# Kernel tuning notes

Measured on AMD Instinct MI355X. Metric: run time of the kernel, lower is better.

Reference implementation:

```python
import jax, jax.numpy as jnp
import numpy as np

B, C, H, W, D = 4, 256, 16, 16, 16
N = H * W * D          # 4096 tokens == input_size
HEADS, P = 8, 64       # num_heads, proj_size
EPS_LN, EPS_BN, NEG_SLOPE = 1e-5, 1e-5, 0.01


def setup_inputs() -> dict:
    key = jax.random.key(0)
    ks = jax.random.split(key, 10)
    s = 0.02
    rn = lambda k, shp: (s * jax.random.normal(k, shp)).astype(jnp.float32)
    return {
        "x": jax.random.normal(ks[0], (B, C, H, W, D), jnp.float32),
        "gamma": 1e-6 * jnp.ones((C,), jnp.float32),
        "ln_w": jnp.ones((C,), jnp.float32),
        "ln_b": jnp.zeros((C,), jnp.float32),
        "qkvv_w": rn(ks[1], (4 * C, C)),          # Linear(C, 4C), bias=False
        "ef_w": rn(ks[2], (P, N)),                 # shared E == F projection
        "ef_b": jnp.zeros((P,), jnp.float32),
        "temp": jnp.ones((HEADS, 1, 1), jnp.float32),
        "temp2": jnp.ones((HEADS, 1, 1), jnp.float32),
        "op1_w": rn(ks[3], (C // 2, C)),
        "op1_b": jnp.zeros((C // 2,), jnp.float32),
        "op2_w": rn(ks[4], (C // 2, C)),
        "op2_b": jnp.zeros((C // 2,), jnp.float32),
        "conv1_w": rn(ks[5], (C, C, 3, 3, 3)),     # UnetResBlock convs, bias=False
        "bn1_w": jnp.ones((C,), jnp.float32),
        "bn1_b": jnp.zeros((C,), jnp.float32),
        "conv2_w": rn(ks[6], (C, C, 3, 3, 3)),
        "bn2_w": jnp.ones((C,), jnp.float32),
        "bn2_b": jnp.zeros((C,), jnp.float32),
        "conv8_w": rn(ks[7], (C, C, 1, 1, 1)),     # nn.Conv3d 1x1x1, bias=True
        "conv8_b": jnp.zeros((C,), jnp.float32),
    }


def _l2norm(t):  # torch F.normalize(dim=-1)
    n = jnp.sqrt(jnp.sum(t * t, axis=-1, keepdims=True))
    return t / jnp.maximum(n, 1e-12)


def _conv3d(x, w, pad):
    return jax.lax.conv_general_dilated(
        x, w, window_strides=(1, 1, 1), padding=[(pad, pad)] * 3,
        dimension_numbers=("NCDHW", "OIDHW", "NCDHW"))


def _bn(x, w, b):  # BatchNorm3d, training-mode batch stats, biased var
    mu = jnp.mean(x, axis=(0, 2, 3, 4), keepdims=True)
    var = jnp.mean((x - mu) ** 2, axis=(0, 2, 3, 4), keepdims=True)
    xh = (x - mu) / jnp.sqrt(var + EPS_BN)
    return xh * w[None, :, None, None, None] + b[None, :, None, None, None]


def _lrelu(x):
    return jnp.where(x >= 0, x, NEG_SLOPE * x)


def _epa(xs, qkvv_w, ef_w, ef_b, temp, temp2, op1_w, op1_b, op2_w, op2_b):
    Bq, Nq, Cq = xs.shape
    d = Cq // HEADS
    qkvv = (xs @ qkvv_w.T).reshape(Bq, Nq, 4, HEADS, d)
    qkvv = jnp.transpose(qkvv, (2, 0, 3, 1, 4))         # (4,B,h,N,d)
    q, k, v_ca, v_sa = qkvv[0], qkvv[1], qkvv[2], qkvv[3]
    q = jnp.swapaxes(q, -2, -1)                          # (B,h,d,N)
    k = jnp.swapaxes(k, -2, -1)
    v_ca = jnp.swapaxes(v_ca, -2, -1)
    v_sa = jnp.swapaxes(v_sa, -2, -1)
    k_proj = k @ ef_w.T + ef_b                           # (B,h,d,P)
    v_sa_proj = v_sa @ ef_w.T + ef_b                     # (B,h,d,P)
    qn = _l2norm(q)
    kn = _l2norm(k)
    # channel attention: (B,h,d,d)
    attn_ca = jax.nn.softmax(jnp.einsum("bhdn,bhen->bhde", qn, kn) * temp, axis=-1)
    x_ca = jnp.einsum("bhde,bhen->bhdn", attn_ca, v_ca)  # (B,h,d,N)
    x_ca = jnp.transpose(x_ca, (0, 3, 1, 2)).reshape(Bq, Nq, Cq)
    # spatial attention with projected K/V: (B,h,N,P)
    attn_sa = jax.nn.softmax(jnp.einsum("bhdn,bhdp->bhnp", qn, k_proj) * temp2, axis=-1)
    x_sa = jnp.einsum("bhnp,bhdp->bhnd", attn_sa, v_sa_proj)   # (B,h,N,d)
    # faithful to source: permute(0,3,1,2) then reshape(B,N,C)
    x_sa = jnp.transpose(x_sa, (0, 3, 1, 2)).reshape(Bq, Nq, Cq)
    x_sa = x_sa @ op1_w.T + op1_b
    x_ca = x_ca @ op2_w.T + op2_b
    return jnp.concatenate((x_sa, x_ca), axis=-1)


def reference(x, gamma, ln_w, ln_b, qkvv_w, ef_w, ef_b, temp, temp2,
              op1_w, op1_b, op2_w, op2_b, conv1_w, bn1_w, bn1_b,
              conv2_w, bn2_w, bn2_b, conv8_w, conv8_b):
    Bq, Cq, Hq, Wq, Dq = x.shape
    Nq = Hq * Wq * Dq
    xs = jnp.transpose(x.reshape(Bq, Cq, Nq), (0, 2, 1))       # (B,N,C)
    mu = jnp.mean(xs, axis=-1, keepdims=True)
    var = jnp.mean((xs - mu) ** 2, axis=-1, keepdims=True)
    xn = (xs - mu) / jnp.sqrt(var + EPS_LN) * ln_w + ln_b
    attn = xs + gamma * _epa(xn, qkvv_w, ef_w, ef_b, temp, temp2,
                             op1_w, op1_b, op2_w, op2_b)
    attn_skip = jnp.transpose(attn.reshape(Bq, Hq, Wq, Dq, Cq), (0, 4, 1, 2, 3))
    # UnetResBlock (identity shortcut: same channels, stride 1)
    h1 = _lrelu(_bn(_conv3d(attn_skip, conv1_w, 1), bn1_w, bn1_b))
    h2 = _bn(_conv3d(h1, conv2_w, 1), bn2_w, bn2_b)
    conv_out = _lrelu(h2 + attn_skip)
    # conv8: Dropout3d (identity in eval) + 1x1x1 conv with bias
    c8 = _conv3d(conv_out, conv8_w, 0) + conv8_b[None, :, None, None, None]
    return attn_skip + c8
```

## Files before the change

kernel.cpp:

```cpp
#include <hip/hip_runtime.h>

#define B_ 4
#define C_ 256
#define N_ 4096

typedef unsigned short u16;
typedef __attribute__((ext_vector_type(8))) short short8_t;
typedef __attribute__((ext_vector_type(4))) float f32x4;

__device__ __forceinline__ u16 bf16r(float f) {
  unsigned u = __float_as_uint(f);
  return (u16)((u + 0x7FFFu + ((u >> 16) & 1u)) >> 16);
}
__device__ __forceinline__ float bf2f(u16 u) {
  return __uint_as_float(((unsigned)u) << 16);
}

__device__ __forceinline__ void g2l16(const u16* g, u16* l) {
  __builtin_amdgcn_global_load_lds((const __attribute__((address_space(1))) void*)g,
                                   (__attribute__((address_space(3))) void*)l, 16, 0, 0);
}

__device__ __forceinline__ int f4(int x) { return (x ^ (x >> 2)) & 3; }

__global__ __launch_bounds__(256) void k_ln(const float* __restrict__ x,
                                            const float* __restrict__ ln_w,
                                            const float* __restrict__ ln_b,
                                            u16* __restrict__ xnb) {
  __shared__ float tile[32][260];
  __shared__ float s_mu[32], s_rs[32];
  int b = blockIdx.y, n0 = blockIdx.x * 32, tid = threadIdx.x;
  for (int idx = tid; idx < 32 * 256; idx += 256) {
    int nl = idx & 31, c = idx >> 5;
    tile[nl][c] = x[((size_t)(b * C_ + c)) * N_ + n0 + nl];
  }
  __syncthreads();
  int token = tid >> 3, sub = tid & 7;
  float s = 0.f, sq = 0.f;
  for (int j = 0; j < 32; ++j) {
    float v = tile[token][sub + j * 8];
    s += v; sq += v * v;
  }
  for (int o = 1; o < 8; o <<= 1) { s += __shfl_xor(s, o); sq += __shfl_xor(sq, o); }
  if (sub == 0) {
    float mu = s * (1.f / 256.f);
    float var = sq * (1.f / 256.f) - mu * mu;
    s_mu[token] = mu;
    s_rs[token] = rsqrtf(var + 1e-5f);
  }
  __syncthreads();
  int c = tid;
  float lw = ln_w[c], lb = ln_b[c];
  for (int k = 0; k < 32; ++k) {
    float v = (tile[k][c] - s_mu[k]) * s_rs[k] * lw + lb;
    xnb[((size_t)(b * N_ + n0 + k)) * 256 + c] = bf16r(v);
  }
}

__global__ __launch_bounds__(256) void k_pack(const float* __restrict__ w,
                                              u16* __restrict__ dst,
                                              int ntap, int K) {
  int tid = threadIdx.x;
  int tile = blockIdx.x;
  int tap = tile % ntap; int tmp = tile / ntap; int Kt = K >> 5;
  int k0 = tmp % Kt; int ot = tmp / Kt;
  u16* td = dst + (size_t)tile * 4096;
  int m = tid >> 1;
  int kb = (tid & 1) * 16;
  int fm = f4(m);
  #pragma unroll
  for (int j = 0; j < 16; ++j) {
    int k = kb + j;
    float v = w[((size_t)(ot * 128 + m) * K + k0 * 32 + k) * ntap + tap];
    td[m * 32 + (((k >> 3) ^ fm) << 3) + (k & 7)] = bf16r(v);
  }
}

__global__ __launch_bounds__(256) void k_packA(const float* __restrict__ w,
                                               u16* __restrict__ dst) {
  int tid = threadIdx.x;
  int tile = blockIdx.x;
  int tap = tile % 27; int tmp = tile / 27;
  int k0 = tmp & 7; int ot = tmp >> 3;
  u16* td = dst + (size_t)tile * 4096;
  int m = tid >> 1;
  int kb = (tid & 1) * 16;
  #pragma unroll
  for (int j = 0; j < 16; ++j) {
    int k = kb + j;
    float v = w[((size_t)(ot * 128 + m) * 256 + k0 * 32 + k) * 27 + tap];
    td[m * 32 + k] = bf16r(v);
  }
}

__global__ __launch_bounds__(64) void k_packef(const float* __restrict__ ef,
                                               u16* __restrict__ dst) {
  int k0 = blockIdx.x, m = threadIdx.x, fm = f4(m);
  u16* td = dst + (size_t)k0 * 2048;
  #pragma unroll
  for (int k = 0; k < 32; ++k)
    td[m * 32 + (((k >> 3) ^ fm) << 3) + (k & 7)] = bf16r(ef[(size_t)m * 4096 + k0 * 32 + k]);
}

__global__ __launch_bounds__(256) void k_gemm(const u16* __restrict__ xnb,
                                              const u16* __restrict__ qpack,
                                              u16* __restrict__ qct,
                                              float* __restrict__ sbuf) {
  __shared__ alignas(16) u16 At[4096];
  __shared__ alignas(16) u16 Bt[4096];
  __shared__ alignas(16) u16 Tt[128 * 136];
  int tid = threadIdx.x, l = tid & 63, w = tid >> 6;
  int wm = w >> 1, wn = w & 1;
  int kg = l >> 4;
  int tok0 = blockIdx.x * 128, oct = blockIdx.y;
  int b = tok0 >> 12;
  int aoff[4], boff[4];
  #pragma unroll
  for (int r = 0; r < 4; ++r) {
    int m = wm * 64 + r * 16 + (l & 15);
    aoff[r] = m * 32 + ((kg ^ f4(m)) << 3);
    int o = wn * 64 + r * 16 + (l & 15);
    boff[r] = o * 32 + ((kg ^ f4(o)) << 3);
  }
  f32x4 acc[4][4];
  #pragma unroll
  for (int r = 0; r < 4; ++r)
    #pragma unroll
    for (int jt = 0; jt < 4; ++jt)
      acc[r][jt] = (f32x4){0.f, 0.f, 0.f, 0.f};
  for (int k0 = 0; k0 < 8; ++k0) {
    __syncthreads();
    #pragma unroll
    for (int it = 0; it < 2; ++it) {
      int slot = it * 256 + tid;
      int row = slot >> 2, cp = slot & 3;
      int cig = cp ^ f4(row);
      g2l16(xnb + ((size_t)(tok0 + row) * 256 + k0 * 32 + cig * 8),
            &At[(it * 256 + (tid & 192)) * 8]);
    }
    const u16* qb = qpack + ((size_t)(oct * 8 + k0) << 12);
    #pragma unroll
    for (int it = 0; it < 2; ++it)
      g2l16(qb + (it * 256 + tid) * 8, &Bt[(it * 256 + (tid & 192)) * 8]);
    __syncthreads();
    short8_t av[4], bv[4];
    #pragma unroll
    for (int r = 0; r < 4; ++r) av[r] = *(const short8_t*)&At[aoff[r]];
    #pragma unroll
    for (int jt = 0; jt < 4; ++jt) bv[jt] = *(const short8_t*)&Bt[boff[jt]];
    #pragma unroll
    for (int r = 0; r < 4; ++r)
      #pragma unroll
      for (int jt = 0; jt < 4; ++jt)
        acc[r][jt] = __builtin_amdgcn_mfma_f32_16x16x32_bf16(av[r], bv[jt], acc[r][jt], 0, 0, 0);
  }
  if (oct < 4) {
    #pragma unroll
    for (int jt = 0; jt < 4; ++jt) {
      float ss = 0.f;
      #pragma unroll
      for (int r = 0; r < 4; ++r)
        #pragma unroll
        for (int reg = 0; reg < 4; ++reg)
          ss += acc[r][jt][reg] * acc[r][jt][reg];
      ss += __shfl_xor(ss, 16);
      ss += __shfl_xor(ss, 32);
      if ((l >> 4) == 0) {
        int oc = oct * 128 + wn * 64 + jt * 16 + (l & 15);
        atomicAdd(&sbuf[(oc >> 8) * 1024 + b * 256 + (oc & 255)], ss);
      }
    }
  }
  #pragma unroll
  for (int r = 0; r < 4; ++r) {
    int tokl = wm * 64 + r * 16 + ((l >> 4) << 2);
    #pragma unroll
    for (int jt = 0; jt < 4; ++jt) {
      int ocl = wn * 64 + jt * 16 + (l & 15);
      ushort4 h4;
      h4.x = bf16r(acc[r][jt][0]);
      h4.y = bf16r(acc[r][jt][1]);
      h4.z = bf16r(acc[r][jt][2]);
      h4.w = bf16r(acc[r][jt][3]);
      *(ushort4*)&Tt[ocl * 136 + tokl] = h4;
    }
  }
  __syncthreads();
  int n0 = tok0 & 4095;
  #pragma unroll
  for (int i = 0; i < 8; ++i) {
    int s = i * 256 + tid;
    int row = s >> 4;
    int col = (s & 15) * 8;
    *(int4*)&qct[((size_t)(b * 1024 + oct * 128 + row)) * 4096 + n0 + col] =
        *(const int4*)&Tt[row * 136 + col];
  }
}

__global__ __launch_bounds__(256) void k_rsq(const float* __restrict__ sbuf,
                                             float* __restrict__ inv) {
  int i = blockIdx.x * 256 + threadIdx.x;
  inv[i] = 1.f / fmaxf(sqrtf(sbuf[i]), 1e-12f);
}

__global__ __launch_bounds__(256) void k_kvproj_m(const u16* __restrict__ qct,
                                                  const u16* __restrict__ efp,
                                                  float* __restrict__ kvpart) {
  __shared__ alignas(16) u16 At[16384];
  __shared__ alignas(16) u16 Bt[8192];
  int tid = threadIdx.x, l = tid & 63, w = tid >> 6;
  int mt = blockIdx.x, b = blockIdx.y, kz = blockIdx.z;
  int ccb = (mt < 2) ? (256 + mt * 128) : (768 + (mt - 2) * 128);
  int kg = l >> 4;
  int aoff[2], boff[4];
  #pragma unroll
  for (int r = 0; r < 2; ++r) {
    int m = w * 32 + r * 16 + (l & 15);
    aoff[r] = m * 32 + ((kg ^ f4(m)) << 3);
  }
  #pragma unroll
  for (int jt = 0; jt < 4; ++jt) {
    int o = jt * 16 + (l & 15);
    boff[jt] = o * 32 + ((kg ^ f4(o)) << 3);
  }
  f32x4 acc[2][4];
  #pragma unroll
  for (int r = 0; r < 2; ++r)
    #pragma unroll
    for (int jt = 0; jt < 4; ++jt) acc[r][jt] = (f32x4){0.f, 0.f, 0.f, 0.f};
  for (int k0 = kz * 8; k0 < kz * 8 + 8; ++k0) {
    __syncthreads();
    #pragma unroll
    for (int it = 0; it < 8; ++it) {
      int slot = it * 256 + tid;
      int sub = slot >> 9, r = (slot >> 2) & 127, cp = slot & 3;
      g2l16(qct + ((size_t)(b * 1024 + ccb + r)) * 4096 + k0 * 128 + sub * 32 + ((cp ^ f4(r)) << 3),
            &At[(it * 256 + (tid & 192)) * 8]);
    }
    #pragma unroll
    for (int it = 0; it < 4; ++it) {
      int slot = it * 256 + tid;
      g2l16(efp + (size_t)k0 * 8192 + slot * 8, &Bt[(it * 256 + (tid & 192)) * 8]);
    }
    __syncthreads();
    #pragma unroll
    for (int sub = 0; sub < 4; ++sub) {
      short8_t av[2], bv[4];
      #pragma unroll
      for (int r = 0; r < 2; ++r) av[r] = *(const short8_t*)&At[sub * 4096 + aoff[r]];
      #pragma unroll
      for (int jt = 0; jt < 4; ++jt) bv[jt] = *(const short8_t*)&Bt[sub * 2048 + boff[jt]];
      #pragma unroll
      for (int r = 0; r < 2; ++r)
        #pragma unroll
        for (int jt = 0; jt < 4; ++jt)
          acc[r][jt] = __builtin_amdgcn_mfma_f32_16x16x32_bf16(av[r], bv[jt], acc[r][jt], 0, 0, 0);
    }
  }
  int kv = mt >> 1;
  float* outd = kvpart + (size_t)kv * 524288 + (size_t)kz * 131072;
  #pragma unroll
  for (int r = 0; r < 2; ++r) {
    int cbase = (mt & 1) * 128 + w * 32 + r * 16 + ((l >> 4) << 2);
    #pragma unroll
    for (int jt = 0; jt < 4; ++jt) {
      int p = jt * 16 + (l & 15);
      #pragma unroll
      for (int reg = 0; reg < 4; ++reg) {
        int cc = cbase + reg;
        outd[((size_t)(b * 8 + (cc >> 5))) * 2048 + (cc & 31) * 64 + p] = acc[r][jt][reg];
      }
    }
  }
}

__global__ __launch_bounds__(256) void k_kvred(const float* __restrict__ kvpart,
                                               const float* __restrict__ ef_b,
                                               float* __restrict__ kproj,
                                               float* __restrict__ vproj) {
  int kv = blockIdx.y;
  int i = (blockIdx.x * 256 + threadIdx.x) * 4;
  const float* p = kvpart + (size_t)kv * 524288 + i;
  float4 a0 = *(const float4*)&p[0];
  float4 a1 = *(const float4*)&p[131072];
  float4 a2 = *(const float4*)&p[262144];
  float4 a3 = *(const float4*)&p[393216];
  int pp = i & 63;
  float4 o;
  o.x = a0.x + a1.x + a2.x + a3.x + ef_b[pp];
  o.y = a0.y + a1.y + a2.y + a3.y + ef_b[pp + 1];
  o.z = a0.z + a1.z + a2.z + a3.z + ef_b[pp + 2];
  o.w = a0.w + a1.w + a2.w + a3.w + ef_b[pp + 3];
  float* outd = kv ? vproj : kproj;
  *(float4*)&outd[i] = o;
}

__global__ __launch_bounds__(256) void k_attnca_p(const u16* __restrict__ qct,
                                                  float* __restrict__ Spp) {
  __shared__ u16 Qs[32][520], Ks[32][520];
  int bh = blockIdx.x, ns = blockIdx.y;
  int b = bh >> 3, h = bh & 7;
  int tid = threadIdx.x;
  int n0 = ns * 512;
  for (int idx = tid; idx < 2048; idx += 256) {
    int r = idx >> 6, ch = (idx & 63) * 8;
    *(int4*)&Qs[r][ch] = *(const int4*)&qct[((size_t)(b * 1024 + h * 32 + r)) * 4096 + n0 + ch];
    *(int4*)&Ks[r][ch] = *(const int4*)&qct[((size_t)(b * 1024 + 256 + h * 32 + r)) * 4096 + n0 + ch];
  }
  __syncthreads();
  int r = tid >> 3, sub = tid & 7;
  float a0 = 0.f, a1 = 0.f, a2 = 0.f, a3 = 0.f;
  for (int nb = 0; nb < 512; nb += 8) {
    short8_t q8 = *(const short8_t*)&Qs[r][nb];
    short8_t k0 = *(const short8_t*)&Ks[sub][nb];
    short8_t k1 = *(const short8_t*)&Ks[sub + 8][nb];
    short8_t k2 = *(const short8_t*)&Ks[sub + 16][nb];
    short8_t k3 = *(const short8_t*)&Ks[sub + 24][nb];
    #pragma unroll
    for (int j = 0; j < 8; ++j) {
      float qv = bf2f((u16)q8[j]);
      a0 += qv * bf2f((u16)k0[j]);
      a1 += qv * bf2f((u16)k1[j]);
      a2 += qv * bf2f((u16)k2[j]);
      a3 += qv * bf2f((u16)k3[j]);
    }
  }
  float* sp = Spp + (size_t)ns * 32768 + (size_t)bh * 1024 + r * 32;
  sp[sub] = a0;
  sp[sub + 8] = a1;
  sp[sub + 16] = a2;
  sp[sub + 24] = a3;
}

__global__ __launch_bounds__(64) void k_casm(const float* __restrict__ Spp,
                                             const float* __restrict__ inv,
                                             const float* __restrict__ temp,
                                             float* __restrict__ Aca) {
  int bh = blockIdx.x, b = bh >> 3, h = bh & 7;
  int tid = threadIdx.x;
  if (tid < 32) {
    float qiv = inv[b * 256 + h * 32 + tid];
    float tmp = temp[h];
    float vals[32];
    #pragma unroll
    for (int e = 0; e < 32; ++e) vals[e] = 0.f;
    for (int ns = 0; ns < 8; ++ns) {
      const float* sp = Spp + (size_t)ns * 32768 + (size_t)bh * 1024 + tid * 32;
      #pragma unroll
      for (int e4 = 0; e4 < 32; e4 += 4) {
        float4 v4 = *(const float4*)&sp[e4];
        vals[e4] += v4.x; vals[e4 + 1] += v4.y;
        vals[e4 + 2] += v4.z; vals[e4 + 3] += v4.w;
      }
    }
    float m = -1e30f;
    #pragma unroll
    for (int e = 0; e < 32; ++e) {
      float s = vals[e] * qiv * inv[1024 + b * 256 + h * 32 + e] * tmp;
      vals[e] = s;
      m = fmaxf(m, s);
    }
    float ssum = 0.f;
    #pragma unroll
    for (int e = 0; e < 32; ++e) { vals[e] = __expf(vals[e] - m); ssum += vals[e]; }
    float is = 1.f / ssum;
    #pragma unroll
    for (int e = 0; e < 32; ++e) Aca[((size_t)bh * 32 + tid) * 32 + e] = vals[e] * is;
  }
}

__global__ __launch_bounds__(256) void k_xca(const u16* __restrict__ qct,
                                             const float* __restrict__ Aca,
                                             u16* __restrict__ xca_b) {
  __shared__ float A[32][33];
  __shared__ float vt[32][129];
  int n0 = blockIdx.x * 128;
  int h = blockIdx.y, b = blockIdx.z;
  int bh = b * 8 + h;
  int tid = threadIdx.x;
  for (int idx = tid; idx < 1024; idx += 256) A[idx >> 5][idx & 31] = Aca[(size_t)bh * 1024 + idx];
  int e = tid >> 3, ns = (tid & 7) * 16;
  const u16* src = qct + ((size_t)(b * 1024 + 512 + h * 32 + e)) * 4096 + n0 + ns;
  #pragma unroll
  for (int j4 = 0; j4 < 16; j4 += 4) {
    ushort4 u = *(const ushort4*)&src[j4];
    vt[e][ns + j4] = bf2f(u.x);
    vt[e][ns + j4 + 1] = bf2f(u.y);
    vt[e][ns + j4 + 2] = bf2f(u.z);
    vt[e][ns + j4 + 3] = bf2f(u.w);
  }
  __syncthreads();
  int nl = tid & 127, dg = (tid >> 7) * 16;
  float acc[16] = {};
  for (int ee = 0; ee < 32; ++ee) {
    float v = vt[ee][nl];
    #pragma unroll
    for (int j = 0; j < 16; ++j) acc[j] += A[dg + j][ee] * v;
  }
  u16* outp = xca_b + ((size_t)(b * N_ + n0 + nl)) * 256 + h * 32 + dg;
  #pragma unroll
  for (int j = 0; j < 16; ++j) outp[j] = bf16r(acc[j]);
}

__global__ __launch_bounds__(256) void k_attnsa(const u16* __restrict__ qct,
                                                const float* __restrict__ kproj,
                                                const float* __restrict__ vproj,
                                                const float* __restrict__ inv,
                                                const float* __restrict__ temp2,
                                                u16* __restrict__ xsa_b) {
  __shared__ float kp[32][64], vp[32][64], qi[32];
  __shared__ u16 qt[32][260];
  __shared__ float ot[32][257];
  int bx = blockIdx.x;
  int h = blockIdx.y, b = blockIdx.z;
  int bh = b * 8 + h;
  int tid = threadIdx.x;
  for (int idx = tid; idx < 2048; idx += 256) {
    kp[idx >> 6][idx & 63] = kproj[(size_t)bh * 2048 + idx];
    vp[idx >> 6][idx & 63] = vproj[(size_t)bh * 2048 + idx];
  }
  if (tid < 32) qi[tid] = inv[bh * 32 + tid];
  {
    int row = tid >> 3, ch = (tid & 7) * 32;
    const u16* src = qct + ((size_t)(b * 1024 + h * 32 + row)) * 4096 + bx * 256 + ch;
    *(int4*)&qt[row][ch] = *(const int4*)&src[0];
    *(int4*)&qt[row][ch + 8] = *(const int4*)&src[8];
    *(int4*)&qt[row][ch + 16] = *(const int4*)&src[16];
    *(int4*)&qt[row][ch + 24] = *(const int4*)&src[24];
  }
  __syncthreads();
  float q[32];
  #pragma unroll
  for (int d = 0; d < 32; ++d) q[d] = bf2f(qt[d][tid]) * qi[d];
  float t2 = temp2[h];
  float l[64];
  #pragma unroll
  for (int p = 0; p < 64; ++p) {
    float s = 0;
    #pragma unroll
    for (int d = 0; d < 32; ++d) s += q[d] * kp[d][p];
    l[p] = s * t2;
  }
  float m = -1e30f;
  #pragma unroll
  for (int p = 0; p < 64; ++p) m = fmaxf(m, l[p]);
  float ssum = 0;
  #pragma unroll
  for (int p = 0; p < 64; ++p) { l[p] = __expf(l[p] - m); ssum += l[p]; }
  float is = 1.f / ssum;
  float o[32] = {};
  #pragma unroll
  for (int p = 0; p < 64; ++p) {
    float wv = l[p] * is;
    #pragma unroll
    for (int d = 0; d < 32; ++d) o[d] += wv * vp[d][p];
  }
  #pragma unroll
  for (int d = 0; d < 32; ++d) ot[d][tid] = o[d];
  __syncthreads();
  #pragma unroll
  for (int i = 0; i < 4; ++i) {
    int s = i * 256 + tid;
    int d = s >> 5;
    int c0 = (s & 31) * 8;
    ushort4 u0, u1;
    u0.x = bf16r(ot[d][c0]);     u0.y = bf16r(ot[d][c0 + 1]);
    u0.z = bf16r(ot[d][c0 + 2]); u0.w = bf16r(ot[d][c0 + 3]);
    u1.x = bf16r(ot[d][c0 + 4]); u1.y = bf16r(ot[d][c0 + 5]);
    u1.z = bf16r(ot[d][c0 + 6]); u1.w = bf16r(ot[d][c0 + 7]);
    u16* dst = xsa_b + (size_t)b * N_ * 256 + (size_t)(d * 128 + h * 16 + bx) * 256 + c0;
    *(ushort4*)&dst[0] = u0;
    *(ushort4*)&dst[4] = u1;
  }
}

__global__ __launch_bounds__(256) void k_opcatm(const u16* __restrict__ xsa_b,
                                                const u16* __restrict__ xca_b,
                                                const float* __restrict__ x,
                                                const float* __restrict__ gamma,
                                                const u16* __restrict__ oppack,
                                                const float* __restrict__ op1_b,
                                                const float* __restrict__ op2_b,
                                                float* __restrict__ attn_skip,
                                                u16* __restrict__ xt1) {
  __shared__ alignas(16) u16 At[4096];
  __shared__ alignas(16) u16 Bt[4096];
  __shared__ alignas(16) float Ttf[128 * 133];
  __shared__ alignas(16) u16 rb[128 * 136];
  int tid = threadIdx.x, l = tid & 63, w = tid >> 6;
  int wm = w >> 1, wn = w & 1;
  int kg = l >> 4;
  int tok0 = blockIdx.x * 128, oct = blockIdx.y;
  int b = tok0 >> 12;
  const u16* src = oct ? xca_b : xsa_b;
  int aoff[4], boff[4];
  #pragma unroll
  for (int r = 0; r < 4; ++r) {
    int m = wm * 64 + r * 16 + (l & 15);
    aoff[r] = m * 32 + ((kg ^ f4(m)) << 3);
    int o = wn * 64 + r * 16 + (l & 15);
    boff[r] = o * 32 + ((kg ^ f4(o)) << 3);
  }
  f32x4 acc[4][4];
  #pragma unroll
// ... 168 lines not shown
    #pragma unroll
    for (int r = 0; r < 4; ++r) av[0][r] = *(const short8_t*)(at + r * 512);
    #pragma unroll
    for (int r = 0; r < 4; ++r) av[1][r] = *(const short8_t*)(at + 4096 + r * 512);
    #pragma unroll
    for (int r = 0; r < 4; ++r) av[2][r] = *(const short8_t*)(at + 8192 + r * 512);
    #pragma unroll
    for (int jt = 0; jt < 4; ++jt) {
      bv[0][jt] = *(const short8_t*)&Xb[(cellc[jt] - 197) * 8];
      bv[1][jt] = *(const short8_t*)&Xb[(cellc[jt] - 196) * 8];
    }
    #pragma unroll
    for (int t = 0; t < 4; ++t) CONV_TAP(t);
    if (step < 3) {
      const int nd = (step + 1) & 1;
      #pragma unroll
      for (int bk = 0; bk < 2; ++bk)
        #pragma unroll
        for (int i = 0; i < 4; ++i) {
          const u16* p = ((okm >> i) & 1) ? (xp[i] + ((bk * 4 + step + 1) << 5)) : zg;
          g2l16(p, &Xs[bk][nd][(i * 256 + (tid & 192)) * 8]);
        }
    }
    #pragma unroll
    for (int t = 4; t < 27; ++t) CONV_TAP(t);
    __syncthreads();
  }
#undef CONV_TAP

  f32x4* red = (f32x4*)&Xs[0][0][0];
  if (ks == 1) {
    #pragma unroll
    for (int r = 0; r < 4; ++r)
      #pragma unroll
      for (int jt = 0; jt < 4; ++jt)
        red[(r * 4 + jt) * 128 + wm * 64 + l] = acc[r][jt];
  }
  __syncthreads();
  if (ks == 0) {
    #pragma unroll
    for (int r = 0; r < 4; ++r)
      #pragma unroll
      for (int jt = 0; jt < 4; ++jt) {
        f32x4 o = red[(r * 4 + jt) * 128 + wm * 64 + l];
        acc[r][jt][0] += o[0]; acc[r][jt][1] += o[1];
        acc[r][jt][2] += o[2]; acc[r][jt][3] += o[3];
      }
    #pragma unroll
    for (int r = 0; r < 4; ++r) {
      int co = cot * 128 + wm * 64 + r * 16 + ((l >> 4) << 2);
      #pragma unroll
      for (int reg = 0; reg < 4; ++reg) {
        float sv = 0.f, qv = 0.f;
        #pragma unroll
        for (int jt = 0; jt < 4; ++jt) {
          float v = acc[r][jt][reg];
          sv += v; qv += v * v;
        }
        #pragma unroll
        for (int o = 1; o < 16; o <<= 1) {
          sv += __shfl_xor(sv, o);
          qv += __shfl_xor(qv, o);
        }
        if ((l & 15) == 0) {
          atomicAdd(&bnsum[co + reg], sv);
          atomicAdd(&bnsq[co + reg], qv);
        }
      }
      #pragma unroll
      for (int jt = 0; jt < 4; ++jt) {
        int c = jt * 16 + (l & 15);
        int n = (h0 + (c >> 4)) * 256 + (w0 + ((c >> 2) & 3)) * 16 + (d0 + (c & 3));
        ushort4 h4;
        h4.x = bf16r(acc[r][jt][0]);
        h4.y = bf16r(acc[r][jt][1]);
        h4.z = bf16r(acc[r][jt][2]);
        h4.w = bf16r(acc[r][jt][3]);
        *(ushort4*)&out[((size_t)(b * N_ + n)) * 256 + co] = h4;
      }
    }
  }
}

__global__ __launch_bounds__(256) void k_bnfin(const float* __restrict__ bnsum,
                                               const float* __restrict__ bnsq,
                                               float* __restrict__ mu,
                                               float* __restrict__ rstd) {
  int c = threadIdx.x;
  float m = bnsum[c] * (1.f / 16384.f);
  float var = bnsq[c] * (1.f / 16384.f) - m * m;
  mu[c] = m;
  rstd[c] = rsqrtf(var + 1e-5f);
}

__global__ __launch_bounds__(256) void k_bnelt(const u16* __restrict__ src,
                                               const float* __restrict__ mu,
                                               const float* __restrict__ rstd,
                                               const float* __restrict__ w,
                                               const float* __restrict__ bb,
                                               u16* __restrict__ dst) {
  __shared__ float sc[256], sh[256];
  int tid = threadIdx.x;
  float scv = rstd[tid] * w[tid];
  sc[tid] = scv;
  sh[tid] = bb[tid] - mu[tid] * scv;
  __syncthreads();
  size_t base = (size_t)blockIdx.x * 64 * 256;
  #pragma unroll
  for (int i = 0; i < 8; ++i) {
    int s = i * 256 + tid;
    int c0 = (s & 31) * 8;
    size_t off = base + (size_t)(s >> 5) * 256 + c0;
    int4 v4 = *(const int4*)&src[off];
    u16* pu = (u16*)&v4;
    #pragma unroll
    for (int j = 0; j < 8; ++j) {
      float v = bf2f(pu[j]) * sc[c0 + j] + sh[c0 + j];
      pu[j] = bf16r(v >= 0.f ? v : 0.01f * v);
    }
    *(int4*)&dst[off] = v4;
  }
}

__global__ __launch_bounds__(256) void k_bn2fuse(const u16* __restrict__ c2o,
                                                 const float* __restrict__ askip,
                                                 const float* __restrict__ mu2,
                                                 const float* __restrict__ rs2,
                                                 const float* __restrict__ bnw,
                                                 const float* __restrict__ bnb,
                                                 u16* __restrict__ cvo) {
  __shared__ float sc[256], sh[256];
  __shared__ float at_[32][260];
  int n0 = blockIdx.x * 32, b = blockIdx.y, tid = threadIdx.x;
  float scv = rs2[tid] * bnw[tid];
  sc[tid] = scv;
  sh[tid] = bnb[tid] - mu2[tid] * scv;
  {
    int c = tid;
    const float* ar = askip + ((size_t)(b * 256 + c)) * 4096 + n0;
    #pragma unroll
    for (int nl = 0; nl < 32; ++nl) at_[nl][c] = ar[nl];
  }
  __syncthreads();
  #pragma unroll
  for (int i = 0; i < 4; ++i) {
    int s = i * 256 + tid;
    int row = s >> 5, c0 = (s & 31) * 8;
    size_t off = ((size_t)(b * N_ + n0 + row)) * 256 + c0;
    int4 v4 = *(const int4*)&c2o[off];
    u16* pu = (u16*)&v4;
    #pragma unroll
    for (int j = 0; j < 8; ++j) {
      int c = c0 + j;
      float v = bf2f(pu[j]) * sc[c] + sh[c] + at_[row][c];
      pu[j] = bf16r(v >= 0.f ? v : 0.01f * v);
    }
    *(int4*)&cvo[off] = v4;
  }
}

__global__ __launch_bounds__(256) void k_conv8m(const u16* __restrict__ cvo,
                                                const u16* __restrict__ w8p,
                                                const float* __restrict__ b8,
                                                const float* __restrict__ skip,
                                                float* __restrict__ out) {
  __shared__ alignas(16) u16 At[4096];
  __shared__ alignas(16) u16 Bt[4096];
  __shared__ alignas(16) float Ts[128 * 132];
  int tid = threadIdx.x, l = tid & 63, w = tid >> 6;
  int wm = w >> 1, wn = w & 1;
  int kg = l >> 4;
  int tok0 = blockIdx.x * 128, oct = blockIdx.y;
  int b = tok0 >> 12;
  int aoff[4], boff[4];
  #pragma unroll
  for (int r = 0; r < 4; ++r) {
    int m = wm * 64 + r * 16 + (l & 15);
    aoff[r] = m * 32 + ((kg ^ f4(m)) << 3);
    int o = wn * 64 + r * 16 + (l & 15);
    boff[r] = o * 32 + ((kg ^ f4(o)) << 3);
  }
  f32x4 acc[4][4];
  #pragma unroll
  for (int r = 0; r < 4; ++r)
    #pragma unroll
    for (int jt = 0; jt < 4; ++jt)
      acc[r][jt] = (f32x4){0.f, 0.f, 0.f, 0.f};
  for (int k0 = 0; k0 < 8; ++k0) {
    __syncthreads();
    #pragma unroll
    for (int it = 0; it < 2; ++it) {
      int slot = it * 256 + tid;
      int row = slot >> 2, cp = slot & 3;
      int cig = cp ^ f4(row);
      g2l16(cvo + ((size_t)(tok0 + row) * 256 + k0 * 32 + cig * 8),
            &At[(it * 256 + (tid & 192)) * 8]);
    }
    const u16* qb = w8p + ((size_t)(oct * 8 + k0) << 12);
    #pragma unroll
    for (int it = 0; it < 2; ++it)
      g2l16(qb + (it * 256 + tid) * 8, &Bt[(it * 256 + (tid & 192)) * 8]);
    __syncthreads();
    short8_t av[4], bv[4];
    #pragma unroll
    for (int r = 0; r < 4; ++r) av[r] = *(const short8_t*)&At[aoff[r]];
    #pragma unroll
    for (int jt = 0; jt < 4; ++jt) bv[jt] = *(const short8_t*)&Bt[boff[jt]];
    #pragma unroll
    for (int r = 0; r < 4; ++r)
      #pragma unroll
      for (int jt = 0; jt < 4; ++jt)
        acc[r][jt] = __builtin_amdgcn_mfma_f32_16x16x32_bf16(av[r], bv[jt], acc[r][jt], 0, 0, 0);
  }
  #pragma unroll
  for (int r = 0; r < 4; ++r) {
    int tokl = wm * 64 + r * 16 + ((l >> 4) << 2);
    #pragma unroll
    for (int jt = 0; jt < 4; ++jt) {
      int ocl = wn * 64 + jt * 16 + (l & 15);
      *(float4*)&Ts[ocl * 132 + tokl] =
          (float4){acc[r][jt][0], acc[r][jt][1], acc[r][jt][2], acc[r][jt][3]};
    }
  }
  __syncthreads();
  int n0l = tok0 & 4095;
  #pragma unroll
  for (int i = 0; i < 16; ++i) {
    int s = i * 256 + tid;
    int row = s >> 5;
    int c4 = (s & 31) * 4;
    int oc = oct * 128 + row;
    size_t base = ((size_t)(b * 256 + oc)) * 4096 + n0l + c4;
    float4 s4 = *(const float4*)&skip[base];
    float bias = b8[oc];
    const float* tp = &Ts[row * 132 + c4];
    float4 o4;
    o4.x = s4.x + bias + tp[0];
    o4.y = s4.y + bias + tp[1];
    o4.z = s4.z + bias + tp[2];
    o4.w = s4.w + bias + tp[3];
    *(float4*)&out[base] = o4;
  }
}

extern "C" void kernel_launch(void* const* d_in, const int* in_sizes, int n_in,
                              void* d_out, int out_size, void* d_ws, size_t ws_size,
                              hipStream_t stream) {
  const float* x       = (const float*)d_in[0];
  const float* gamma   = (const float*)d_in[1];
  const float* ln_w    = (const float*)d_in[2];
  const float* ln_b    = (const float*)d_in[3];
  const float* qkvv_w  = (const float*)d_in[4];
  const float* ef_w    = (const float*)d_in[5];
  const float* ef_b    = (const float*)d_in[6];
  const float* temp    = (const float*)d_in[7];
  const float* temp2   = (const float*)d_in[8];
  const float* op1_w   = (const float*)d_in[9];
  const float* op1_b   = (const float*)d_in[10];
  const float* op2_w   = (const float*)d_in[11];
  const float* op2_b   = (const float*)d_in[12];
  const float* conv1_w = (const float*)d_in[13];
  const float* bn1_w   = (const float*)d_in[14];
  const float* bn1_b   = (const float*)d_in[15];
  const float* conv2_w = (const float*)d_in[16];
  const float* bn2_w   = (const float*)d_in[17];
  const float* bn2_b   = (const float*)d_in[18];
  const float* conv8_w = (const float*)d_in[19];
  const float* conv8_b = (const float*)d_in[20];

  float* ws = (float*)d_ws;
  const size_t M1 = 1u << 20;
  float* askip  = ws;
  u16*   xt1    = (u16*)(ws + 16 * M1);
  u16*   xnb    = (u16*)(ws + 18 * M1);
  float* kvpart = ws + 18 * M1;
  float* Spp    = ws + 19 * M1;
  u16*   xsa_b  = (u16*)(ws + 18 * M1);
  u16*   xca_b  = (u16*)(ws + 22 * M1);
  u16*   cvo    = (u16*)(ws + 22 * M1);
  u16*   qct    = (u16*)(ws + 24 * M1);
  u16*   apack1 = (u16*)(ws + 24 * M1);
  u16*   apack2 = (u16*)(ws + 25 * M1);
  u16*   c1o    = (u16*)(ws + 26 * M1);
  u16*   ht     = (u16*)(ws + 28 * M1);
  u16*   c2o    = (u16*)(ws + 30 * M1);
  float* sm     = ws + 32 * M1;
  float* sbuf   = sm;
  float* qkinv  = sbuf + 2048;
  float* kproj  = qkinv + 2048;
  float* vproj  = kproj + 65536;
  float* Sp     = vproj + 65536;
  float* bnacc  = Sp + 32768;
  float* zgu_f  = bnacc + 1024;
  u16*   zgu    = (u16*)zgu_f;
  float* Aca    = zgu_f + 128;
  float* mu1    = Aca + 32768;
  float* rs1    = mu1 + 256;
  float* mu2    = rs1 + 256;
  float* rs2    = mu2 + 256;
  u16*   qpack  = (u16*)(rs2 + 256);
  u16*   efpack = (u16*)(rs2 + 256 + 131072);
  u16*   w8pack = (u16*)(rs2 + 256 + 262144);
  u16*   oppack = (u16*)(rs2 + 256 + 262144 + 32768);

  hipMemsetAsync(sbuf, 0, 2048 * 4, stream);
  hipMemsetAsync(bnacc, 0, (1024 + 128) * 4, stream);
  k_pack<<<dim3(64), 256, 0, stream>>>(qkvv_w, qpack, 1, 256);
  k_pack<<<dim3(16), 256, 0, stream>>>(conv8_w, w8pack, 1, 256);
  k_pack<<<dim3(8), 256, 0, stream>>>(op1_w, oppack, 1, 256);
  k_pack<<<dim3(8), 256, 0, stream>>>(op2_w, oppack + 32768, 1, 256);
  k_packef<<<dim3(128), 64, 0, stream>>>(ef_w, efpack);
  k_ln<<<dim3(128, 4), 256, 0, stream>>>(x, ln_w, ln_b, xnb);
  k_gemm<<<dim3(128, 8), 256, 0, stream>>>(xnb, qpack, qct, sbuf);
  k_rsq<<<dim3(8), 256, 0, stream>>>(sbuf, qkinv);
  k_kvproj_m<<<dim3(4, 4, 4), 256, 0, stream>>>(qct, efpack, kvpart);
  k_kvred<<<dim3(64, 2), 256, 0, stream>>>(kvpart, ef_b, kproj, vproj);
  k_attnca_p<<<dim3(32, 8), 256, 0, stream>>>(qct, Spp);
  k_casm<<<dim3(32), 64, 0, stream>>>(Spp, qkinv, temp, Aca);
  k_xca<<<dim3(32, 8, 4), 256, 0, stream>>>(qct, Aca, xca_b);
  k_attnsa<<<dim3(16, 8, 4), 256, 0, stream>>>(qct, kproj, vproj, qkinv, temp2, xsa_b);
  k_opcatm<<<dim3(128, 2), 256, 0, stream>>>(xsa_b, xca_b, x, gamma, oppack, op1_b, op2_b, askip, xt1);
  k_packA<<<dim3(432), 256, 0, stream>>>(conv1_w, apack1);
  k_packA<<<dim3(432), 256, 0, stream>>>(conv2_w, apack2);
  k_conv3m<<<dim3(512), 256, 0, stream>>>(xt1, apack1, zgu, c1o, bnacc, bnacc + 256);
  k_bnfin<<<1, 256, 0, stream>>>(bnacc, bnacc + 256, mu1, rs1);
  k_bnelt<<<dim3(256), 256, 0, stream>>>(c1o, mu1, rs1, bn1_w, bn1_b, ht);
  k_conv3m<<<dim3(512), 256, 0, stream>>>(ht, apack2, zgu, c2o, bnacc + 512, bnacc + 768);
  k_bnfin<<<1, 256, 0, stream>>>(bnacc + 512, bnacc + 768, mu2, rs2);
  k_bn2fuse<<<dim3(128, 4), 256, 0, stream>>>(c2o, askip, mu2, rs2, bn2_w, bn2_b, cvo);
  k_conv8m<<<dim3(128, 2), 256, 0, stream>>>(cvo, w8pack, conv8_b, askip, (float*)d_out);
}
```

Baseline: 353.5 us.

## Merge weight-pack kernels and fold small reduction kernels into consumers

Combines all weight packing into one k_prepack launch and merges the two memsets into one. Removes the small kernels k_rsq, k_kvred, k_casm and k_bnfin by recomputing their results inside the consuming kernels (k_xca, k_attnsa, k_bnelt, k_bn2fuse). The workspace layout is rearranged so apack1/apack2 do not alias qct and can be packed up front. The intent is to cut launch count and serialization gaps, at the cost of redundant per-block recomputation such as the softmax and kv reduction in every k_xca block.

```diff
diff --git a/kernel.cpp b/kernel.cpp
--- a/kernel.cpp
+++ b/kernel.cpp
@@ -57,49 +57,60 @@
   }
 }
 
-__global__ __launch_bounds__(256) void k_pack(const float* __restrict__ w,
-                                              u16* __restrict__ dst,
-                                              int ntap, int K) {
-  int tid = threadIdx.x;
-  int tile = blockIdx.x;
-  int tap = tile % ntap; int tmp = tile / ntap; int Kt = K >> 5;
-  int k0 = tmp % Kt; int ot = tmp / Kt;
-  u16* td = dst + (size_t)tile * 4096;
-  int m = tid >> 1;
-  int kb = (tid & 1) * 16;
-  int fm = f4(m);
-  #pragma unroll
-  for (int j = 0; j < 16; ++j) {
-    int k = kb + j;
-    float v = w[((size_t)(ot * 128 + m) * K + k0 * 32 + k) * ntap + tap];
-    td[m * 32 + (((k >> 3) ^ fm) << 3) + (k & 7)] = bf16r(v);
-  }
-}
-
-__global__ __launch_bounds__(256) void k_packA(const float* __restrict__ w,
-                                               u16* __restrict__ dst) {
-  int tid = threadIdx.x;
-  int tile = blockIdx.x;
-  int tap = tile % 27; int tmp = tile / 27;
-  int k0 = tmp & 7; int ot = tmp >> 3;
-  u16* td = dst + (size_t)tile * 4096;
-  int m = tid >> 1;
-  int kb = (tid & 1) * 16;
-  #pragma unroll
-  for (int j = 0; j < 16; ++j) {
-    int k = kb + j;
-    float v = w[((size_t)(ot * 128 + m) * 256 + k0 * 32 + k) * 27 + tap];
-    td[m * 32 + k] = bf16r(v);
-  }
-}
-
-__global__ __launch_bounds__(64) void k_packef(const float* __restrict__ ef,
-                                               u16* __restrict__ dst) {
-  int k0 = blockIdx.x, m = threadIdx.x, fm = f4(m);
-  u16* td = dst + (size_t)k0 * 2048;
-  #pragma unroll
-  for (int k = 0; k < 32; ++k)
-    td[m * 32 + (((k >> 3) ^ fm) << 3) + (k & 7)] = bf16r(ef[(size_t)m * 4096 + k0 * 32 + k]);
+__global__ __launch_bounds__(256) void k_prepack(const float* __restrict__ qkvv_w,
+                                                 const float* __restrict__ conv8_w,
+                                                 const float* __restrict__ op1_w,
+                                                 const float* __restrict__ op2_w,
+                                                 const float* __restrict__ ef_w,
+                                                 const float* __restrict__ conv1_w,
+                                                 const float* __restrict__ conv2_w,
+                                                 u16* __restrict__ qpack,
+                                                 u16* __restrict__ w8pack,
+                                                 u16* __restrict__ oppack,
+                                                 u16* __restrict__ efpack,
+                                                 u16* __restrict__ apack1,
+                                                 u16* __restrict__ apack2) {
+  int bid = blockIdx.x, tid = threadIdx.x;
+  if (bid < 96) {
+    const float* w; u16* dst; int tile;
+    if (bid < 64)      { w = qkvv_w;  dst = qpack;          tile = bid; }
+    else if (bid < 80) { w = conv8_w; dst = w8pack;         tile = bid - 64; }
+    else if (bid < 88) { w = op1_w;   dst = oppack;         tile = bid - 80; }
+    else               { w = op2_w;   dst = oppack + 32768; tile = bid - 88; }
+    int k0 = tile & 7, ot = tile >> 3;
+    u16* td = dst + (size_t)tile * 4096;
+    int m = tid >> 1, kb = (tid & 1) * 16, fm = f4(m);
+    #pragma unroll
+    for (int j = 0; j < 16; ++j) {
+      int k = kb + j;
+      float v = w[(size_t)(ot * 128 + m) * 256 + k0 * 32 + k];
+      td[m * 32 + (((k >> 3) ^ fm) << 3) + (k & 7)] = bf16r(v);
+    }
+  } else if (bid < 224) {
+    int k0 = bid - 96;
+    int m = tid & 63, kq = tid >> 6, fm = f4(m);
+    u16* td = efpack + (size_t)k0 * 2048;
+    #pragma unroll
+    for (int kk = 0; kk < 8; ++kk) {
+      int k = kq * 8 + kk;
+      td[m * 32 + (((k >> 3) ^ fm) << 3) + (k & 7)] = bf16r(ef_w[(size_t)m * 4096 + k0 * 32 + k]);
+    }
+  } else {
+    int t = bid - 224;
+    const float* w = (t < 432) ? conv1_w : conv2_w;
+    u16* dst = (t < 432) ? apack1 : apack2;
+    int tile = (t < 432) ? t : t - 432;
+    int tap = tile % 27; int tmp = tile / 27;
+    int k0 = tmp & 7; int ot = tmp >> 3;
+    u16* td = dst + (size_t)tile * 4096;
+    int m = tid >> 1, kb = (tid & 1) * 16;
+    #pragma unroll
+    for (int j = 0; j < 16; ++j) {
+      int k = kb + j;
+      float v = w[((size_t)(ot * 128 + m) * 256 + k0 * 32 + k) * 27 + tap];
+      td[m * 32 + k] = bf16r(v);
+    }
+  }
 }
 
 __global__ __launch_bounds__(256) void k_gemm(const u16* __restrict__ xnb,
@@ -197,12 +208,6 @@
   }
 }
 
-__global__ __launch_bounds__(256) void k_rsq(const float* __restrict__ sbuf,
-                                             float* __restrict__ inv) {
-  int i = blockIdx.x * 256 + threadIdx.x;
-  inv[i] = 1.f / fmaxf(sqrtf(sbuf[i]), 1e-12f);
-}
-
 __global__ __launch_bounds__(256) void k_kvproj_m(const u16* __restrict__ qct,
                                                   const u16* __restrict__ efp,
                                                   float* __restrict__ kvpart) {
@@ -272,27 +277,6 @@
       }
     }
   }
-}
-
-__global__ __launch_bounds__(256) void k_kvred(const float* __restrict__ kvpart,
-                                               const float* __restrict__ ef_b,
-                                               float* __restrict__ kproj,
-                                               float* __restrict__ vproj) {
-  int kv = blockIdx.y;
-  int i = (blockIdx.x * 256 + threadIdx.x) * 4;
-  const float* p = kvpart + (size_t)kv * 524288 + i;
-  float4 a0 = *(const float4*)&p[0];
-  float4 a1 = *(const float4*)&p[131072];
-  float4 a2 = *(const float4*)&p[262144];
-  float4 a3 = *(const float4*)&p[393216];
-  int pp = i & 63;
-  float4 o;
-  o.x = a0.x + a1.x + a2.x + a3.x + ef_b[pp];
-  o.y = a0.y + a1.y + a2.y + a3.y + ef_b[pp + 1];
-  o.z = a0.z + a1.z + a2.z + a3.z + ef_b[pp + 2];
-  o.w = a0.w + a1.w + a2.w + a3.w + ef_b[pp + 3];
-  float* outd = kv ? vproj : kproj;
-  *(float4*)&outd[i] = o;
 }
 
 __global__ __launch_bounds__(256) void k_attnca_p(const u16* __restrict__ qct,
@@ -332,45 +316,10 @@
   sp[sub + 24] = a3;
 }
 
-__global__ __launch_bounds__(64) void k_casm(const float* __restrict__ Spp,
-                                             const float* __restrict__ inv,
+__global__ __launch_bounds__(256) void k_xca(const u16* __restrict__ qct,
+                                             const float* __restrict__ Spp,
+                                             const float* __restrict__ sbuf,
                                              const float* __restrict__ temp,
-                                             float* __restrict__ Aca) {
-  int bh = blockIdx.x, b = bh >> 3, h = bh & 7;
-  int tid = threadIdx.x;
-  if (tid < 32) {
-    float qiv = inv[b * 256 + h * 32 + tid];
-    float tmp = temp[h];
-    float vals[32];
-    #pragma unroll
-    for (int e = 0; e < 32; ++e) vals[e] = 0.f;
-    for (int ns = 0; ns < 8; ++ns) {
-      const float* sp = Spp + (size_t)ns * 32768 + (size_t)bh * 1024 + tid * 32;
-      #pragma unroll
-      for (int e4 = 0; e4 < 32; e4 += 4) {
-        float4 v4 = *(const float4*)&sp[e4];
-        vals[e4] += v4.x; vals[e4 + 1] += v4.y;
-        vals[e4 + 2] += v4.z; vals[e4 + 3] += v4.w;
-      }
-    }
-    float m = -1e30f;
-    #pragma unroll
-    for (int e = 0; e < 32; ++e) {
-      float s = vals[e] * qiv * inv[1024 + b * 256 + h * 32 + e] * tmp;
-      vals[e] = s;
-      m = fmaxf(m, s);
-    }
-    float ssum = 0.f;
-    #pragma unroll
-    for (int e = 0; e < 32; ++e) { vals[e] = __expf(vals[e] - m); ssum += vals[e]; }
-    float is = 1.f / ssum;
-    #pragma unroll
-    for (int e = 0; e < 32; ++e) Aca[((size_t)bh * 32 + tid) * 32 + e] = vals[e] * is;
-  }
-}
-
-__global__ __launch_bounds__(256) void k_xca(const u16* __restrict__ qct,
-                                             const float* __restrict__ Aca,
                                              u16* __restrict__ xca_b) {
   __shared__ float A[32][33];
   __shared__ float vt[32][129];
@@ -378,7 +327,36 @@
   int h = blockIdx.y, b = blockIdx.z;
   int bh = b * 8 + h;
   int tid = threadIdx.x;
-  for (int idx = tid; idx < 1024; idx += 256) A[idx >> 5][idx & 31] = Aca[(size_t)bh * 1024 + idx];
+  if (tid < 32) {
+    float qiv = 1.f / fmaxf(sqrtf(sbuf[b * 256 + h * 32 + tid]), 1e-12f);
+    float tmp = temp[h];
+    float vals[32];
+    #pragma unroll
+    for (int e = 0; e < 32; ++e) vals[e] = 0.f;
+    for (int ns = 0; ns < 8; ++ns) {
+      const float* sp = Spp + (size_t)ns * 32768 + (size_t)bh * 1024 + tid * 32;
+      #pragma unroll
+      for (int e4 = 0; e4 < 32; e4 += 4) {
+        float4 v4 = *(const float4*)&sp[e4];
+        vals[e4] += v4.x; vals[e4 + 1] += v4.y;
+        vals[e4 + 2] += v4.z; vals[e4 + 3] += v4.w;
+      }
+    }
+    float mx = -1e30f;
+    #pragma unroll
+    for (int e = 0; e < 32; ++e) {
+      float kiv = 1.f / fmaxf(sqrtf(sbuf[1024 + b * 256 + h * 32 + e]), 1e-12f);
+      float s = vals[e] * qiv * kiv * tmp;
+      vals[e] = s;
+      mx = fmaxf(mx, s);
+    }
+    float ssum = 0.f;
+    #pragma unroll
+    for (int e = 0; e < 32; ++e) { vals[e] = __expf(vals[e] - mx); ssum += vals[e]; }
+    float is = 1.f / ssum;
+    #pragma unroll
+    for (int e = 0; e < 32; ++e) A[tid][e] = vals[e] * is;
+  }
   int e = tid >> 3, ns = (tid & 7) * 16;
   const u16* src = qct + ((size_t)(b * 1024 + 512 + h * 32 + e)) * 4096 + n0 + ns;
   #pragma unroll
@@ -403,9 +381,9 @@
 }
 
 __global__ __launch_bounds__(256) void k_attnsa(const u16* __restrict__ qct,
-                                                const float* __restrict__ kproj,
-                                                const float* __restrict__ vproj,
-                                                const float* __restrict__ inv,
+                                                const float* __restrict__ kvpart,
+                                                const float* __restrict__ ef_b,
+                                                const float* __restrict__ sbuf,
                                                 const float* __restrict__ temp2,
                                                 u16* __restrict__ xsa_b) {
   __shared__ float kp[32][64], vp[32][64], qi[32];
@@ -416,10 +394,18 @@
   int bh = b * 8 + h;
   int tid = threadIdx.x;
   for (int idx = tid; idx < 2048; idx += 256) {
-    kp[idx >> 6][idx & 63] = kproj[(size_t)bh * 2048 + idx];
-    vp[idx >> 6][idx & 63] = vproj[(size_t)bh * 2048 + idx];
-  }
-  if (tid < 32) qi[tid] = inv[bh * 32 + tid];
+    float bias = ef_b[idx & 63];
+    float kpv = bias, vpv = bias;
+    size_t base = (size_t)bh * 2048 + idx;
+    #pragma unroll
+    for (int kz = 0; kz < 4; ++kz) {
+      kpv += kvpart[(size_t)kz * 131072 + base];
+      vpv += kvpart[524288 + (size_t)kz * 131072 + base];
+    }
+    kp[idx >> 6][idx & 63] = kpv;
+    vp[idx >> 6][idx & 63] = vpv;
+  }
+  if (tid < 32) qi[tid] = 1.f / fmaxf(sqrtf(sbuf[b * 256 + h * 32 + tid]), 1e-12f);
   {
     int row = tid >> 3, ch = (tid & 7) * 32;
     const u16* src = qct + ((size_t)(b * 1024 + h * 32 + row)) * 4096 + bx * 256 + ch;
@@ -754,28 +740,20 @@
   }
 }
 
-__global__ __launch_bounds__(256) void k_bnfin(const float* __restrict__ bnsum,
+__global__ __launch_bounds__(256) void k_bnelt(const u16* __restrict__ src,
+                                               const float* __restrict__ bnsum,
                                                const float* __restrict__ bnsq,
-                                               float* __restrict__ mu,
-                                               float* __restrict__ rstd) {
-  int c = threadIdx.x;
-  float m = bnsum[c] * (1.f / 16384.f);
-  float var = bnsq[c] * (1.f / 16384.f) - m * m;
-  mu[c] = m;
-  rstd[c] = rsqrtf(var + 1e-5f);
-}
-
-__global__ __launch_bounds__(256) void k_bnelt(const u16* __restrict__ src,
-                                               const float* __restrict__ mu,
-                                               const float* __restrict__ rstd,
                                                const float* __restrict__ w,
                                                const float* __restrict__ bb,
                                                u16* __restrict__ dst) {
   __shared__ float sc[256], sh[256];
   int tid = threadIdx.x;
-  float scv = rstd[tid] * w[tid];
+  float m = bnsum[tid] * (1.f / 16384.f);
+  float var = bnsq[tid] * (1.f / 16384.f) - m * m;
+  float rstd = rsqrtf(var + 1e-5f);
+  float scv = rstd * w[tid];
   sc[tid] = scv;
-  sh[tid] = bb[tid] - mu[tid] * scv;
+  sh[tid] = bb[tid] - m * scv;
   __syncthreads();
   size_t base = (size_t)blockIdx.x * 64 * 256;
   #pragma unroll
@@ -796,17 +774,20 @@
 
 __global__ __launch_bounds__(256) void k_bn2fuse(const u16* __restrict__ c2o,
                                                  const float* __restrict__ askip,
-                                                 const float* __restrict__ mu2,
-                                                 const float* __restrict__ rs2,
+                                                 const float* __restrict__ bnsum,
+                                                 const float* __restrict__ bnsq,
                                                  const float* __restrict__ bnw,
                                                  const float* __restrict__ bnb,
                                                  u16* __restrict__ cvo) {
   __shared__ float sc[256], sh[256];
   __shared__ float at_[32][260];
   int n0 = blockIdx.x * 32, b = blockIdx.y, tid = threadIdx.x;
-  float scv = rs2[tid] * bnw[tid];
+  float m = bnsum[tid] * (1.f / 16384.f);
+  float var = bnsq[tid] * (1.f / 16384.f) - m * m;
+  float rstd = rsqrtf(var + 1e-5f);
+  float scv = rstd * bnw[tid];
   sc[tid] = scv;
-  sh[tid] = bnb[tid] - mu2[tid] * scv;
+  sh[tid] = bnb[tid] - m * scv;
   {
     int c = tid;
     const float* ar = askip + ((size_t)(b * 256 + c)) * 4096 + n0;
@@ -943,62 +924,43 @@
   float* ws = (float*)d_ws;
   const size_t M1 = 1u << 20;
   float* askip  = ws;
+  u16*   apack1 = (u16*)(ws + 8 * M1);
+  u16*   apack2 = (u16*)(ws + 10 * M1);
   u16*   xt1    = (u16*)(ws + 16 * M1);
   u16*   xnb    = (u16*)(ws + 18 * M1);
-  float* kvpart = ws + 18 * M1;
+  u16*   xsa_b  = (u16*)(ws + 18 * M1);
   float* Spp    = ws + 19 * M1;
-  u16*   xsa_b  = (u16*)(ws + 18 * M1);
+  float* kvpart = ws + 20 * M1;
   u16*   xca_b  = (u16*)(ws + 22 * M1);
   u16*   cvo    = (u16*)(ws + 22 * M1);
   u16*   qct    = (u16*)(ws + 24 * M1);
-  u16*   apack1 = (u16*)(ws + 24 * M1);
-  u16*   apack2 = (u16*)(ws + 25 * M1);
   u16*   c1o    = (u16*)(ws + 26 * M1);
   u16*   ht     = (u16*)(ws + 28 * M1);
   u16*   c2o    = (u16*)(ws + 30 * M1);
   float* sm     = ws + 32 * M1;
   float* sbuf   = sm;
-  float* qkinv  = sbuf + 2048;
-  float* kproj  = qkinv + 2048;
-  float* vproj  = kproj + 65536;
-  float* Sp     = vproj + 65536;
-  float* bnacc  = Sp + 32768;
-  float* zgu_f  = bnacc + 1024;
+  float* bnacc  = sm + 2048;
+  float* zgu_f  = sm + 3072;
   u16*   zgu    = (u16*)zgu_f;
-  float* Aca    = zgu_f + 128;
-  float* mu1    = Aca + 32768;
-  float* rs1    = mu1 + 256;
-  float* mu2    = rs1 + 256;
-  float* rs2    = mu2 + 256;
-  u16*   qpack  = (u16*)(rs2 + 256);
-  u16*   efpack = (u16*)(rs2 + 256 + 131072);
-  u16*   w8pack = (u16*)(rs2 + 256 + 262144);
-  u16*   oppack = (u16*)(rs2 + 256 + 262144 + 32768);
-
-  hipMemsetAsync(sbuf, 0, 2048 * 4, stream);
-  hipMemsetAsync(bnacc, 0, (1024 + 128) * 4, stream);
-  k_pack<<<dim3(64), 256, 0, stream>>>(qkvv_w, qpack, 1, 256);
-  k_pack<<<dim3(16), 256, 0, stream>>>(conv8_w, w8pack, 1, 256);
-  k_pack<<<dim3(8), 256, 0, stream>>>(op1_w, oppack, 1, 256);
-  k_pack<<<dim3(8), 256, 0, stream>>>(op2_w, oppack + 32768, 1, 256);
-  k_packef<<<dim3(128), 64, 0, stream>>>(ef_w, efpack);
+  u16*   qpack  = (u16*)(sm + 3200);
+  u16*   efpack = (u16*)(sm + 3200 + 131072);
+  u16*   w8pack = (u16*)(sm + 3200 + 262144);
+  u16*   oppack = (u16*)(sm + 3200 + 294912);
+
+  hipMemsetAsync(sm, 0, (2048 + 1024 + 128) * 4, stream);
+  k_prepack<<<dim3(1088), 256, 0, stream>>>(qkvv_w, conv8_w, op1_w, op2_w, ef_w,
+                                            conv1_w, conv2_w,
+                                            qpack, w8pack, oppack, efpack, apack1, apack2);
   k_ln<<<dim3(128, 4), 256, 0, stream>>>(x, ln_w, ln_b, xnb);
   k_gemm<<<dim3(128, 8), 256, 0, stream>>>(xnb, qpack, qct, sbuf);
-  k_rsq<<<dim3(8), 256, 0, stream>>>(sbuf, qkinv);
   k_kvproj_m<<<dim3(4, 4, 4), 256, 0, stream>>>(qct, efpack, kvpart);
-  k_kvred<<<dim3(64, 2), 256, 0, stream>>>(kvpart, ef_b, kproj, vproj);
   k_attnca_p<<<dim3(32, 8), 256, 0, stream>>>(qct, Spp);
-  k_casm<<<dim3(32), 64, 0, stream>>>(Spp, qkinv, temp, Aca);
-  k_xca<<<dim3(32, 8, 4), 256, 0, stream>>>(qct, Aca, xca_b);
-  k_attnsa<<<dim3(16, 8, 4), 256, 0, stream>>>(qct, kproj, vproj, qkinv, temp2, xsa_b);
+  k_xca<<<dim3(32, 8, 4), 256, 0, stream>>>(qct, Spp, sbuf, temp, xca_b);
+  k_attnsa<<<dim3(16, 8, 4), 256, 0, stream>>>(qct, kvpart, ef_b, sbuf, temp2, xsa_b);
   k_opcatm<<<dim3(128, 2), 256, 0, stream>>>(xsa_b, xca_b, x, gamma, oppack, op1_b, op2_b, askip, xt1);
-  k_packA<<<dim3(432), 256, 0, stream>>>(conv1_w, apack1);
-  k_packA<<<dim3(432), 256, 0, stream>>>(conv2_w, apack2);
   k_conv3m<<<dim3(512), 256, 0, stream>>>(xt1, apack1, zgu, c1o, bnacc, bnacc + 256);
-  k_bnfin<<<1, 256, 0, stream>>>(bnacc, bnacc + 256, mu1, rs1);
-  k_bnelt<<<dim3(256), 256, 0, stream>>>(c1o, mu1, rs1, bn1_w, bn1_b, ht);
+  k_bnelt<<<dim3(256), 256, 0, stream>>>(c1o, bnacc, bnacc + 256, bn1_w, bn1_b, ht);
   k_conv3m<<<dim3(512), 256, 0, stream>>>(ht, apack2, zgu, c2o, bnacc + 512, bnacc + 768);
-  k_bnfin<<<1, 256, 0, stream>>>(bnacc + 512, bnacc + 768, mu2, rs2);
-  k_bn2fuse<<<dim3(128, 4), 256, 0, stream>>>(c2o, askip, mu2, rs2, bn2_w, bn2_b, cvo);
+  k_bn2fuse<<<dim3(128, 4), 256, 0, stream>>>(c2o, askip, bnacc + 512, bnacc + 768, bn2_w, bn2_b, cvo);
   k_conv8m<<<dim3(128, 2), 256, 0, stream>>>(cvo, w8pack, conv8_b, askip, (float*)d_out);
 }
```

Measured after the change: 328.2 us. 7.1% less time.
